# Performance work log

Measured on AMD Instinct MI355X. Metric: run time of the kernel, lower is better.

## Reference

```python
import jax, jax.numpy as jnp
import numpy as np

BUCKETS = 64
DIM = 512  # self.dim, used only for attention scaling


def setup_inputs() -> dict:
    key = jax.random.key(0)
    k1, k2, k3, k4 = jax.random.split(key, 4)
    b, h, t, dh = 4, 8, 8192, 64
    q = jax.random.normal(k1, (b, h, t, dh), dtype=jnp.float32)
    k = jax.random.normal(k2, (b, h, t, dh), dtype=jnp.float32)
    v = jax.random.normal(k3, (b, h, t, dh), dtype=jnp.float32)
    W = jax.random.normal(k4, (1, h, 2 * dh, BUCKETS), dtype=jnp.float32)  # SimpleSortNet.linear
    return {"q": q, "k": k, "v": v, "W": W}


def reference(q, k, v, W):
    b, h, t, dh = q.shape
    bh = b * h
    bsz = t // BUCKETS  # bucket size = 128

    # merge batch and heads, then bucket: [bh, buckets, bsz, dh]
    b_q = q.reshape(bh, BUCKETS, bsz, dh)
    b_k = k.reshape(bh, BUCKETS, bsz, dh)
    b_v = v.reshape(bh, BUCKETS, bsz, dh)

    # --- SimpleSortNet (non_permutative=True -> softmax, no gumbel) ---
    # summarize each bucket by sum over tokens, concat q/k summaries
    x = jnp.concatenate([b_q.sum(axis=2), b_k.sum(axis=2)], axis=-1)  # [bh, buckets, 2*dh]
    Wb = jnp.broadcast_to(W, (b, h, 2 * dh, BUCKETS)).reshape(bh, 2 * dh, BUCKETS)
    R = jax.nn.relu(jnp.einsum('bud,bdv->buv', x, Wb))  # [bh, buckets, buckets]
    R = jax.nn.softmax(R, axis=-1)

    # zero_all_but_top: keep only top-1 entry along last dim (dim=2)
    top_idx = jnp.argmax(R, axis=-1)  # [bh, buckets]
    top_mask = jnp.arange(BUCKETS) == top_idx[..., None]
    R = jnp.where(top_mask, R, jnp.zeros((), dtype=R.dtype))

    # reorder key/value buckets by (sparsified) R
    b_k_r = jnp.einsum('buv,bvtd->butd', R, b_k)
    b_v_r = jnp.einsum('buv,bvtd->butd', R, b_v)

    # buckets == kv_buckets: attend over [reordered bucket ; own bucket]
    bk = jnp.concatenate([b_k_r, b_k], axis=2)  # [bh, buckets, 2*bsz, dh]
    bv = jnp.concatenate([b_v_r, b_v], axis=2)

    # bucketed attention; note: original scales by self.dim ** -0.5 (full dim)
    dots = jnp.einsum('buie,buje->buij', b_q, bk) * (DIM ** -0.5)
    attn = jax.nn.softmax(dots, axis=-1)
    out = jnp.einsum('buij,buje->buie', attn, bv)  # [bh, buckets, bsz, dh]

    return out.reshape(b, h, t, dh)
```

## Files before the change

kernel.cpp:

```cpp
#include <hip/hip_runtime.h>


#define T_TOK 8192
#define CQ (0.04419417382415922f * 1.4426950408889634f)
#define FIXED_M 12.0f

#define KB_OFF 0
#define VT_OFF 16384
#define XB_OFF 32768
#define QP_OFF 33280
#define KP_OFF 34304

typedef __attribute__((ext_vector_type(16))) float f32x16;
typedef __attribute__((ext_vector_type(8))) short bf16x8;

__device__ __forceinline__ unsigned cvtpk(float lo, float hi) {
  unsigned r;
  asm("v_cvt_pk_bf16_f32 %0, %1, %2" : "=v"(r) : "v"(lo), "v"(hi));
  return r;
}
__device__ __forceinline__ float exp2v(float x) {
  float r;
  asm("v_exp_f32 %0, %1\n\ts_nop 0" : "=v"(r) : "v"(x));
  return r;
}

#define ATTN_TILE(TLOC, VUHALF)                                                \
  {                                                                            \
    int tokr = (TLOC) * 32 + ln;                                               \
    f32x16 acc;                                                                \
    _Pragma("unroll") for (int r = 0; r < 16; ++r) acc[r] = 0.f;               \
    _Pragma("unroll") for (int sl = 0; sl < 4; ++sl) {                         \
      int addr =                                                               \
          KB_OFF + tokr * 128 + ((sl * 32 + lhi * 16) ^ ((tokr & 7) << 4));    \
      bf16x8 af = *reinterpret_cast<const bf16x8*>(smem + addr);               \
      acc = __builtin_amdgcn_mfma_f32_32x32x16_bf16(af, qf[sl], acc, 0, 0, 0); \
    }                                                                          \
    _Pragma("unroll") for (int r = 0; r < 16; ++r) {                           \
      float lg = (VUHALF) ? acc[r] * ru : acc[r];                              \
      float p = exp2v(lg - FIXED_M);                                           \
      acc[r] = p;                                                              \
      lsum += p;                                                               \
    }                                                                          \
    _Pragma("unroll") for (int ks = 0; ks < 2; ++ks) {                         \
      int r0 = 8 * ks;                                                         \
      unsigned aA, bA, aB, bB;                                                 \
      asm("v_cvt_pk_bf16_f32 %0, %1, %2"                                       \
          : "=v"(aA) : "v"(acc[r0 + 0]), "v"(acc[r0 + 1]));                    \
      asm("v_cvt_pk_bf16_f32 %0, %1, %2"                                       \
          : "=v"(bA) : "v"(acc[r0 + 2]), "v"(acc[r0 + 3]));                    \
      asm("v_cvt_pk_bf16_f32 %0, %1, %2"                                       \
          : "=v"(aB) : "v"(acc[r0 + 4]), "v"(acc[r0 + 5]));                    \
      asm("v_cvt_pk_bf16_f32 %0, %1, %2"                                       \
          : "=v"(bB) : "v"(acc[r0 + 6]), "v"(acc[r0 + 7]));                    \
      asm("s_nop 1\n\tv_permlane32_swap_b32 %0, %1\n\ts_nop 1"                 \
          : "+v"(aA), "+v"(aB));                                               \
      asm("s_nop 1\n\tv_permlane32_swap_b32 %0, %1\n\ts_nop 1"                 \
          : "+v"(bA), "+v"(bB));                                               \
      union { unsigned uu[4]; bf16x8 f; } pf;                                  \
      pf.uu[0] = aA; pf.uu[1] = bA; pf.uu[2] = aB; pf.uu[3] = bB;              \
      int t2 = 2 * ((TLOC) * 32 + ks * 16 + lhi * 8);                          \
      {                                                                        \
        int d = ln;                                                            \
        int addr = VT_OFF + d * 256 + (t2 ^ ((d & 15) << 4));                  \
        bf16x8 vf = *reinterpret_cast<const bf16x8*>(smem + addr);             \
        o0 = __builtin_amdgcn_mfma_f32_32x32x16_bf16(pf.f, vf, o0, 0, 0, 0);   \
      }                                                                        \
      {                                                                        \
        int d = 32 + ln;                                                       \
        int addr = VT_OFF + d * 256 + (t2 ^ ((d & 15) << 4));                  \
        bf16x8 vf = *reinterpret_cast<const bf16x8*>(smem + addr);             \
        o1 = __builtin_amdgcn_mfma_f32_32x32x16_bf16(pf.f, vf, o1, 0, 0, 0);   \
      }                                                                        \
    }                                                                          \
  }

__global__ __launch_bounds__(256, 2) void k3_attn(
    const float* __restrict__ q, const float* __restrict__ k,
    const float* __restrict__ v, const float* __restrict__ W,
    float* __restrict__ out) {
  __shared__ unsigned char smem[38400];

  int L = blockIdx.x;
  int G = ((L & 7) << 8) | (L >> 3);
  int bhi = G >> 6, u = G & 63;
  int tid = threadIdx.x;
  int l = tid & 63;
  int w = tid >> 6;
  int lhi = l >> 5;
  int ln = l & 31;
  int hh = bhi & 7;

  const float* kb = k + (size_t)bhi * (T_TOK * 64);
  const float* vb = v + (size_t)bhi * (T_TOK * 64);

  const float* qrow = q + ((size_t)bhi * T_TOK + (size_t)u * 128 + w * 32 + ln) * 64;
  bf16x8 qf[4];
  float qs[32];
  #pragma unroll
  for (int sl = 0; sl < 4; ++sl) {
    float4 a4 = *reinterpret_cast<const float4*>(qrow + sl * 16 + lhi * 8);
    float4 b4 = *reinterpret_cast<const float4*>(qrow + sl * 16 + lhi * 8 + 4);
    qs[sl * 8 + 0] = a4.x; qs[sl * 8 + 1] = a4.y;
    qs[sl * 8 + 2] = a4.z; qs[sl * 8 + 3] = a4.w;
    qs[sl * 8 + 4] = b4.x; qs[sl * 8 + 5] = b4.y;
    qs[sl * 8 + 6] = b4.z; qs[sl * 8 + 7] = b4.w;
    union { unsigned uu[4]; bf16x8 f; } qu;
    qu.uu[0] = cvtpk(a4.x * CQ, a4.y * CQ);
    qu.uu[1] = cvtpk(a4.z * CQ, a4.w * CQ);
    qu.uu[2] = cvtpk(b4.x * CQ, b4.y * CQ);
    qu.uu[3] = cvtpk(b4.z * CQ, b4.w * CQ);
    qf[sl] = qu.f;
  }
  #pragma unroll
  for (int off = 1; off < 32; off <<= 1) {
    #pragma unroll
    for (int j = 0; j < 32; ++j) qs[j] += __shfl_xor(qs[j], off, 64);
  }
  if (ln == 0) {
    float* qp = (float*)(smem + QP_OFF) + w * 64 + lhi * 8;
    #pragma unroll
    for (int sl = 0; sl < 4; ++sl) {
      #pragma unroll
      for (int j = 0; j < 8; ++j) qp[sl * 16 + j] = qs[sl * 8 + j];
    }
  }

  int c4 = tid & 15;
  float4 ksum = make_float4(0.f, 0.f, 0.f, 0.f);
  #pragma unroll
  for (int it = 0; it < 8; ++it) {
    int row = (tid >> 4) + it * 16;
    float4 val = *reinterpret_cast<const float4*>(
        kb + (size_t)(u * 128 + row) * 64 + c4 * 4);
    ksum.x += val.x; ksum.y += val.y; ksum.z += val.z; ksum.w += val.w;
    int addr = KB_OFF + row * 128 + ((c4 * 8) ^ ((row & 7) << 4));
    *reinterpret_cast<uint2*>(smem + addr) =
        make_uint2(cvtpk(val.x, val.y), cvtpk(val.z, val.w));
  }
  *reinterpret_cast<float4*>(smem + KP_OFF + tid * 16) = ksum;

  int tp = tid >> 2;
  {
    const float* s0 = vb + ((size_t)(u * 128 + 2 * tp)) * 64 + (tid & 3) * 4;
    #pragma unroll
    for (int i = 0; i < 4; ++i) {
      int dq = (tid & 3) + 4 * i;
      float4 va = *reinterpret_cast<const float4*>(s0 + i * 16);
      float4 vc = *reinterpret_cast<const float4*>(s0 + i * 16 + 64);
      int t2 = 4 * tp;
      const float* fa = (const float*)&va;
      const float* fc = (const float*)&vc;
      #pragma unroll
      for (int jj = 0; jj < 4; ++jj) {
        int d = dq * 4 + jj;
        int addr = VT_OFF + d * 256 + (t2 ^ ((d & 15) << 4));
        *reinterpret_cast<unsigned*>(smem + addr) = cvtpk(fa[jj], fc[jj]);
      }
    }
  }

  __syncthreads();

  if (tid < 64) {
    const float* qp = (const float*)(smem + QP_OFF);
    float xq = qp[tid] + qp[64 + tid] + qp[128 + tid] + qp[192 + tid];
    const float* kp = (const float*)(smem + KP_OFF);
    float xk = 0.f;
    #pragma unroll
    for (int g = 0; g < 16; ++g) xk += kp[(g * 16 + (tid >> 2)) * 4 + (tid & 3)];
    float* xbw = (float*)(smem + XB_OFF);
    xbw[tid] = xq;
    xbw[64 + tid] = xk;
  }
  __syncthreads();

  const float* xb = (const float*)(smem + XB_OFF);
  const float* wcol = W + (size_t)hh * 8192 + l;
  float a = 0.f;
  #pragma unroll 8
  for (int kk = 0; kk < 128; ++kk) a = fmaf(xb[kk], wcol[(size_t)kk * 64], a);
  a = fmaxf(a, 0.f);
  float bvv = a; int bi = l;
  #pragma unroll
  for (int off = 1; off < 64; off <<= 1) {
    float ov = __shfl_xor(bvv, off, 64);
    int oi = __shfl_xor(bi, off, 64);
    if (ov > bvv || (ov == bvv && oi < bi)) { bvv = ov; bi = oi; }
  }
  float e = __expf(a - bvv);
  #pragma unroll
  for (int off = 1; off < 64; off <<= 1) e += __shfl_xor(e, off, 64);
  int vu = bi;
  float ru = 1.f / e;

  float4 kvu[8];
  #pragma unroll
  for (int it = 0; it < 8; ++it) {
    int row = (tid >> 4) + it * 16;
    kvu[it] = *reinterpret_cast<const float4*>(
        kb + (size_t)(vu * 128 + row) * 64 + c4 * 4);
  }
  float4 vvu[8];
  {
    const float* s0 = vb + ((size_t)(vu * 128 + 2 * tp)) * 64 + (tid & 3) * 4;
    #pragma unroll
    for (int i = 0; i < 4; ++i) {
      vvu[i] = *reinterpret_cast<const float4*>(s0 + i * 16);
      vvu[4 + i] = *reinterpret_cast<const float4*>(s0 + i * 16 + 64);
    }
  }

  f32x16 o0, o1;
  #pragma unroll
  for (int r = 0; r < 16; ++r) { o0[r] = 0.f; o1[r] = 0.f; }
  float lsum = 0.f;

  #pragma unroll
  for (int t8 = 0; t8 < 4; ++t8) ATTN_TILE(t8, false)

  __syncthreads();

  #pragma unroll
  for (int it = 0; it < 8; ++it) {
    int row = (tid >> 4) + it * 16;
    int addr = KB_OFF + row * 128 + ((c4 * 8) ^ ((row & 7) << 4));
    *reinterpret_cast<uint2*>(smem + addr) =
        make_uint2(cvtpk(kvu[it].x, kvu[it].y), cvtpk(kvu[it].z, kvu[it].w));
  }
  #pragma unroll
  for (int i = 0; i < 4; ++i) {
    int dq = (tid & 3) + 4 * i;
    int t2 = 4 * tp;
    const float* fa = (const float*)&vvu[i];
    const float* fc = (const float*)&vvu[4 + i];
    #pragma unroll
    for (int jj = 0; jj < 4; ++jj) {
      int d = dq * 4 + jj;
      int addr = VT_OFF + d * 256 + (t2 ^ ((d & 15) << 4));
      *reinterpret_cast<unsigned*>(smem + addr) = cvtpk(fa[jj] * ru, fc[jj] * ru);
    }
  }
  __syncthreads();

  #pragma unroll
  for (int t8 = 0; t8 < 4; ++t8) ATTN_TILE(t8, true)

  lsum += __shfl_xor(lsum, 32, 64);
  float inv = 1.f / lsum;
  float* ob = out + ((size_t)bhi * T_TOK + (size_t)u * 128 + w * 32) * 64;
  #pragma unroll
  for (int r = 0; r < 16; ++r) {
    int row = (r & 3) + 8 * (r >> 2) + 4 * lhi;
    float invr = __shfl(inv, row, 64);
    ob[(size_t)row * 64 + ln] = o0[r] * invr;
    ob[(size_t)row * 64 + 32 + ln] = o1[r] * invr;
  }
}

extern "C" void kernel_launch(void* const* d_in, const int* in_sizes, int n_in,
                              void* d_out, int out_size, void* d_ws, size_t ws_size,
                              hipStream_t stream) {
  const float* q = (const float*)d_in[0];
  const float* k = (const float*)d_in[1];
  const float* v = (const float*)d_in[2];
  const float* W = (const float*)d_in[3];
  float* out = (float*)d_out;

  hipLaunchKernelGGL(k3_attn, dim3(2048), dim3(256), 0, stream, q, k, v, W, out);
}
```

Before: 78.01 us.

## Hoist all q/k/v global loads upfront and split prologue reductions

Issues all q, k and v float4 global loads at the start of the kernel into registers, so their latencies overlap instead of being serialized with conversion and LDS stores. It also splits the q-summary and k-summary reductions across two waves instead of one. The W matvec now uses four independent accumulators, fully unrolled, to shorten the FMA dependency chain. Keeping 24 float4 values live raises register pressure, which could hurt occupancy under launch_bounds(256,2). The split accumulators also change float summation order slightly.

```diff
diff --git a/kernel.cpp b/kernel.cpp
--- a/kernel.cpp
+++ b/kernel.cpp
@@ -93,14 +93,38 @@
 
   const float* kb = k + (size_t)bhi * (T_TOK * 64);
   const float* vb = v + (size_t)bhi * (T_TOK * 64);
+  int c4 = tid & 15;
+  int tp = tid >> 2;
 
   const float* qrow = q + ((size_t)bhi * T_TOK + (size_t)u * 128 + w * 32 + ln) * 64;
+  float4 qld[8];
+  #pragma unroll
+  for (int sl = 0; sl < 4; ++sl) {
+    qld[2 * sl] = *reinterpret_cast<const float4*>(qrow + sl * 16 + lhi * 8);
+    qld[2 * sl + 1] = *reinterpret_cast<const float4*>(qrow + sl * 16 + lhi * 8 + 4);
+  }
+  float4 kld[8];
+  #pragma unroll
+  for (int it = 0; it < 8; ++it) {
+    int row = (tid >> 4) + it * 16;
+    kld[it] = *reinterpret_cast<const float4*>(
+        kb + (size_t)(u * 128 + row) * 64 + c4 * 4);
+  }
+  float4 vld[8];
+  {
+    const float* s0 = vb + ((size_t)(u * 128 + 2 * tp)) * 64 + (tid & 3) * 4;
+    #pragma unroll
+    for (int i = 0; i < 4; ++i) {
+      vld[i] = *reinterpret_cast<const float4*>(s0 + i * 16);
+      vld[4 + i] = *reinterpret_cast<const float4*>(s0 + i * 16 + 64);
+    }
+  }
+
   bf16x8 qf[4];
   float qs[32];
   #pragma unroll
   for (int sl = 0; sl < 4; ++sl) {
-    float4 a4 = *reinterpret_cast<const float4*>(qrow + sl * 16 + lhi * 8);
-    float4 b4 = *reinterpret_cast<const float4*>(qrow + sl * 16 + lhi * 8 + 4);
+    float4 a4 = qld[2 * sl], b4 = qld[2 * sl + 1];
     qs[sl * 8 + 0] = a4.x; qs[sl * 8 + 1] = a4.y;
     qs[sl * 8 + 2] = a4.z; qs[sl * 8 + 3] = a4.w;
     qs[sl * 8 + 4] = b4.x; qs[sl * 8 + 5] = b4.y;
@@ -126,61 +150,61 @@
     }
   }
 
-  int c4 = tid & 15;
   float4 ksum = make_float4(0.f, 0.f, 0.f, 0.f);
   #pragma unroll
   for (int it = 0; it < 8; ++it) {
-    int row = (tid >> 4) + it * 16;
-    float4 val = *reinterpret_cast<const float4*>(
-        kb + (size_t)(u * 128 + row) * 64 + c4 * 4);
+    float4 val = kld[it];
     ksum.x += val.x; ksum.y += val.y; ksum.z += val.z; ksum.w += val.w;
+    int row = (tid >> 4) + it * 16;
     int addr = KB_OFF + row * 128 + ((c4 * 8) ^ ((row & 7) << 4));
     *reinterpret_cast<uint2*>(smem + addr) =
         make_uint2(cvtpk(val.x, val.y), cvtpk(val.z, val.w));
   }
   *reinterpret_cast<float4*>(smem + KP_OFF + tid * 16) = ksum;
 
-  int tp = tid >> 2;
-  {
-    const float* s0 = vb + ((size_t)(u * 128 + 2 * tp)) * 64 + (tid & 3) * 4;
-    #pragma unroll
-    for (int i = 0; i < 4; ++i) {
-      int dq = (tid & 3) + 4 * i;
-      float4 va = *reinterpret_cast<const float4*>(s0 + i * 16);
-      float4 vc = *reinterpret_cast<const float4*>(s0 + i * 16 + 64);
-      int t2 = 4 * tp;
-      const float* fa = (const float*)&va;
-      const float* fc = (const float*)&vc;
+  #pragma unroll
+  for (int i = 0; i < 4; ++i) {
+    int dq = (tid & 3) + 4 * i;
+    int t2 = 4 * tp;
+    const float* fa = (const float*)&vld[i];
+    const float* fc = (const float*)&vld[4 + i];
+    #pragma unroll
+    for (int jj = 0; jj < 4; ++jj) {
+      int d = dq * 4 + jj;
+      int addr = VT_OFF + d * 256 + (t2 ^ ((d & 15) << 4));
+      *reinterpret_cast<unsigned*>(smem + addr) = cvtpk(fa[jj], fc[jj]);
+    }
+  }
+
+  __syncthreads();
+
+  if (tid < 128) {
+    float* xbw = (float*)(smem + XB_OFF);
+    if (tid < 64) {
+      const float* qp = (const float*)(smem + QP_OFF);
+      xbw[tid] = qp[tid] + qp[64 + tid] + qp[128 + tid] + qp[192 + tid];
+    } else {
+      int d = tid - 64;
+      const float* kp = (const float*)(smem + KP_OFF);
+      float xk = 0.f;
       #pragma unroll
-      for (int jj = 0; jj < 4; ++jj) {
-        int d = dq * 4 + jj;
-        int addr = VT_OFF + d * 256 + (t2 ^ ((d & 15) << 4));
-        *reinterpret_cast<unsigned*>(smem + addr) = cvtpk(fa[jj], fc[jj]);
-      }
-    }
-  }
-
-  __syncthreads();
-
-  if (tid < 64) {
-    const float* qp = (const float*)(smem + QP_OFF);
-    float xq = qp[tid] + qp[64 + tid] + qp[128 + tid] + qp[192 + tid];
-    const float* kp = (const float*)(smem + KP_OFF);
-    float xk = 0.f;
-    #pragma unroll
-    for (int g = 0; g < 16; ++g) xk += kp[(g * 16 + (tid >> 2)) * 4 + (tid & 3)];
-    float* xbw = (float*)(smem + XB_OFF);
-    xbw[tid] = xq;
-    xbw[64 + tid] = xk;
+      for (int g = 0; g < 16; ++g) xk += kp[(g * 16 + (d >> 2)) * 4 + (d & 3)];
+      xbw[64 + d] = xk;
+    }
   }
   __syncthreads();
 
   const float* xb = (const float*)(smem + XB_OFF);
   const float* wcol = W + (size_t)hh * 8192 + l;
-  float a = 0.f;
-  #pragma unroll 8
-  for (int kk = 0; kk < 128; ++kk) a = fmaf(xb[kk], wcol[(size_t)kk * 64], a);
-  a = fmaxf(a, 0.f);
+  float a0 = 0.f, a1 = 0.f, a2 = 0.f, a3 = 0.f;
+  #pragma unroll
+  for (int kk = 0; kk < 128; kk += 4) {
+    a0 = fmaf(xb[kk + 0], wcol[(size_t)(kk + 0) * 64], a0);
+    a1 = fmaf(xb[kk + 1], wcol[(size_t)(kk + 1) * 64], a1);
+    a2 = fmaf(xb[kk + 2], wcol[(size_t)(kk + 2) * 64], a2);
+    a3 = fmaf(xb[kk + 3], wcol[(size_t)(kk + 3) * 64], a3);
+  }
+  float a = fmaxf((a0 + a1) + (a2 + a3), 0.f);
   float bvv = a; int bi = l;
   #pragma unroll
   for (int off = 1; off < 64; off <<= 1) {
```

After: 68.13 us. -12.7%, faster.
